# Optimization experiments

Measured on AMD Instinct MI355X. Metric: run time of the kernel, lower is better.

The kernel has to match this reference:

```python
import jax, jax.numpy as jnp
import numpy as np

B, H, C, N, K_TERMS = 256, 512, 64, 100, 8


def eval_cubic_spline(coeffs, tobs, t):
    # coeffs: [B, N-1, 4, C]; tobs: [N] sorted knots; t: scalar
    idx = jnp.clip(jnp.searchsorted(tobs, t, side='right') - 1, 0, tobs.shape[0] - 2)
    dt = t - tobs[idx]
    c = coeffs[:, idx]  # [B, 4, C]
    # Horner evaluation: c0 + c1*dt + c2*dt^2 + c3*dt^3
    return c[:, 0] + dt * (c[:, 1] + dt * (c[:, 2] + dt * c[:, 3]))


def setup_inputs() -> dict:
    key = jax.random.key(0)
    k_h, k_c, k_dc, k_wx, k_wh, k_wo = jax.random.split(key, 6)
    xav = lambda k, shape: jax.random.uniform(
        k, shape, minval=-1.0, maxval=1.0, dtype=jnp.float32
    ) * np.float32(np.sqrt(6.0 / (shape[0] + shape[1])))
    return {
        't': jnp.float32(0.5),
        'h': jax.random.normal(k_h, (B, H), dtype=jnp.float32),
        'coeffs': jax.random.normal(k_c, (B, N - 1, 4, C), dtype=jnp.float32),
        'dcoeffs': jax.random.normal(k_dc, (B, N - 1, 4, C), dtype=jnp.float32),
        'tobs': jnp.linspace(0.0, 1.0, N, dtype=jnp.float32),
        'wx': xav(k_wx, (H, C)),
        'wh': xav(k_wh, (H, H)),
        'wout': xav(k_wo, (H, H)),
        'b0': jnp.zeros((H,), dtype=jnp.float32),
        'b1': jnp.zeros((H,), dtype=jnp.float32),
    }


def reference(t, h, coeffs, dcoeffs, tobs, wx, wh, wout, b0, b1):
    x = eval_cubic_spline(coeffs, tobs, t)      # [B, C]
    xdot = eval_cubic_spline(dcoeffs, tobs, t)  # [B, C]
    l1 = x @ wx.T + h @ wh.T + b0               # [B, H]
    relu = jnp.maximum(l1, 0.0)
    th = jnp.tanh(relu @ wout.T + b1)           # [B, H]
    dtanh = 1.0 - th * th
    drelu = jax.nn.sigmoid(l1)                  # surrogate_relu branch
    # Jacobian assembly via broadcasted outer product: [B, H, H]
    d_outer = dtanh[:, :, None] * wout[None, :, :] * drelu[:, None, :]
    Jx = d_outer @ wx                           # [B, H, C]
    Jh = d_outer @ wh                           # [B, H, H]
    curr = jnp.einsum('bhc,bc->bh', Jx, xdot)   # jx matvec, [B, H]
    h_dot = curr
    for _ in range(K_TERMS):                    # Neumann-series recurrence
        curr = jnp.einsum('bij,bj->bi', Jh, curr)
        h_dot = h_dot + curr
    return h_dot
```

## Files before the change

### kernel.cpp

```cpp
#include <hip/hip_runtime.h>

#define BB 256
#define HH 512
#define CC 64
#define NN 100
#define KT 8

typedef short s16x8 __attribute__((ext_vector_type(8)));
typedef float f32x4 __attribute__((ext_vector_type(4)));

#define MFMA16(a, b, c) __builtin_amdgcn_mfma_f32_16x16x32_bf16((a), (b), (c), 0, 0, 0)

static __device__ __forceinline__ unsigned short f2bf(float f) {
    union { float f; unsigned int u; } v; v.f = f;
    unsigned int r = v.u + 0x7FFFu + ((v.u >> 16) & 1u);
    return (unsigned short)(r >> 16);
}


__global__ void k_pack(const float* __restrict__ wh, const float* __restrict__ wout,
                       const float* __restrict__ wx, const float* __restrict__ h,
                       const float* __restrict__ coeffs, const float* __restrict__ dcoeffs,
                       const float* __restrict__ tobs, const float* __restrict__ tg,
                       unsigned short* __restrict__ whp, unsigned short* __restrict__ wop,
                       unsigned short* __restrict__ wxp, unsigned short* __restrict__ hb,
                       unsigned short* __restrict__ xb, unsigned short* __restrict__ xdb,
                       unsigned int* __restrict__ cnt) {
    int gid = blockIdx.x * 256 + threadIdx.x;
    if (gid < 524288) {
        const float* src = (gid < 262144) ? wh : wout;
        unsigned short* dst = (gid < 262144) ? whp : wop;
        int p = gid & 262143;
        int e = p & 7, lane = (p >> 3) & 63, g = (p >> 9) & 15, cg = (p >> 13) & 1, w = p >> 14;
        int row = w * 32 + cg * 16 + (lane & 15);
        int k = g * 32 + (lane >> 4) * 8 + e;
        dst[p] = f2bf(src[row * HH + k]);
    } else if (gid < 557056) {
        int p = gid - 524288;
        int e = p & 7, lane = (p >> 3) & 63, g = (p >> 9) & 1, cg = (p >> 10) & 1, w = p >> 11;
        int row = w * 32 + cg * 16 + (lane & 15);
        int k = g * 32 + (lane >> 4) * 8 + e;
        wxp[p] = f2bf(wx[row * CC + k]);
    } else if (gid < 688128) {
        int p = gid - 557056;
        hb[p] = f2bf(h[p]);
    } else if (gid < 704512) {
        int p = gid - 688128;
        int b = p >> 6, c = p & 63;
        float t = tg[0];
        int cntv = 0;
        for (int n = 0; n < NN; n++) cntv += (tobs[n] <= t) ? 1 : 0;
        int idx = cntv - 1;
        idx = idx < 0 ? 0 : (idx > NN - 2 ? NN - 2 : idx);
        float dt = t - tobs[idx];
        const float* cb = coeffs + ((size_t)(b * (NN - 1) + idx) * 4) * CC + c;
        float xv = cb[0] + dt * (cb[CC] + dt * (cb[2 * CC] + dt * cb[3 * CC]));
        const float* db = dcoeffs + ((size_t)(b * (NN - 1) + idx) * 4) * CC + c;
        float xd = db[0] + dt * (db[CC] + dt * (db[2 * CC] + dt * db[3 * CC]));
        xb[p] = f2bf(xv);
        xdb[p] = f2bf(xd);
    } else if (gid < 704768) {
        cnt[gid - 704512] = 0u;
    }
}

__global__ void k_l1(const unsigned short* __restrict__ whp, const unsigned short* __restrict__ wxp,
                     const unsigned short* __restrict__ hb, const unsigned short* __restrict__ xb,
                     const unsigned short* __restrict__ xdb, const float* __restrict__ b0g,
                     unsigned short* __restrict__ relu_b, float* __restrict__ drelu_f,
                     unsigned short* __restrict__ s0_b) {
    __shared__ unsigned short sh[32][520];
    __shared__ unsigned short sx[32][72];
    __shared__ unsigned short sxd[32][72];
    int tid = threadIdx.x;
    int b0 = blockIdx.x * 32;
    int it = blockIdx.y;
    for (int idx = tid; idx < 32 * 64; idx += 256) {
        int r = idx >> 6, c8 = idx & 63;
        *(int4*)&sh[r][c8 * 8] = *(const int4*)&hb[(b0 + r) * HH + c8 * 8];
    }
    for (int idx = tid; idx < 32 * 8; idx += 256) {
        int r = idx >> 3, c8 = idx & 7;
        *(int4*)&sx[r][c8 * 8] = *(const int4*)&xb[(b0 + r) * CC + c8 * 8];
        *(int4*)&sxd[r][c8 * 8] = *(const int4*)&xdb[(b0 + r) * CC + c8 * 8];
    }
    __syncthreads();
    int wv = tid >> 6, lane = tid & 63, col = lane & 15, kq = lane >> 4;
    int isub = it * 64 + wv * 16;
    int wpk = isub >> 5, cg = (isub >> 4) & 1;
    f32x4 acc0 = {0.f, 0.f, 0.f, 0.f}, acc1 = {0.f, 0.f, 0.f, 0.f};
    f32x4 vac0 = {0.f, 0.f, 0.f, 0.f}, vac1 = {0.f, 0.f, 0.f, 0.f};
    const s16x8* whfrag = (const s16x8*)whp + (size_t)((wpk * 2 + cg) * 16) * 64 + lane;
#pragma unroll
    for (int g = 0; g < 16; g++) {
        s16x8 bf = whfrag[g * 64];
        s16x8 a0 = *(const s16x8*)&sh[col][g * 32 + kq * 8];
        s16x8 a1 = *(const s16x8*)&sh[16 + col][g * 32 + kq * 8];
        acc0 = MFMA16(a0, bf, acc0);
        acc1 = MFMA16(a1, bf, acc1);
    }
    const s16x8* wxfrag = (const s16x8*)wxp + (size_t)((wpk * 2 + cg) * 2) * 64 + lane;
#pragma unroll
    for (int g = 0; g < 2; g++) {
        s16x8 bf = wxfrag[g * 64];
        s16x8 a0 = *(const s16x8*)&sx[col][g * 32 + kq * 8];
        s16x8 a1 = *(const s16x8*)&sx[16 + col][g * 32 + kq * 8];
        acc0 = MFMA16(a0, bf, acc0);
        acc1 = MFMA16(a1, bf, acc1);
        s16x8 d0 = *(const s16x8*)&sxd[col][g * 32 + kq * 8];
        s16x8 d1 = *(const s16x8*)&sxd[16 + col][g * 32 + kq * 8];
        vac0 = MFMA16(d0, bf, vac0);
        vac1 = MFMA16(d1, bf, vac1);
    }
    int ic = isub + col;
    float bias = b0g[ic];
#pragma unroll
    for (int r = 0; r < 4; r++) {
        int bb = b0 + kq * 4 + r;
        float l1a = acc0[r] + bias;
        float dra = 1.f / (1.f + expf(-l1a));
        relu_b[bb * HH + ic] = f2bf(fmaxf(l1a, 0.f));
        drelu_f[bb * HH + ic] = dra;
        s0_b[bb * HH + ic] = f2bf(dra * vac0[r]);
        float l1b = acc1[r] + bias;
        float drb = 1.f / (1.f + expf(-l1b));
        relu_b[(bb + 16) * HH + ic] = f2bf(fmaxf(l1b, 0.f));
        drelu_f[(bb + 16) * HH + ic] = drb;
        s0_b[(bb + 16) * HH + ic] = f2bf(drb * vac1[r]);
    }
}

__global__ void k_th(const unsigned short* __restrict__ wop, const unsigned short* __restrict__ relu_b,
                     const unsigned short* __restrict__ s0_b, const float* __restrict__ b1g,
                     float* __restrict__ dtanh_f, unsigned short* __restrict__ curr_b,
                     float* __restrict__ curr0_f) {
    __shared__ unsigned short sr[32][520];
    __shared__ unsigned short ss0[32][520];
    int tid = threadIdx.x;
    int b0 = blockIdx.x * 32;
    int it = blockIdx.y;
    for (int idx = tid; idx < 32 * 64; idx += 256) {
        int r = idx >> 6, c8 = idx & 63;
        *(int4*)&sr[r][c8 * 8] = *(const int4*)&relu_b[(b0 + r) * HH + c8 * 8];
        *(int4*)&ss0[r][c8 * 8] = *(const int4*)&s0_b[(b0 + r) * HH + c8 * 8];
    }
    __syncthreads();
    int wv = tid >> 6, lane = tid & 63, col = lane & 15, kq = lane >> 4;
    int isub = it * 64 + wv * 16;
    int wpk = isub >> 5, cg = (isub >> 4) & 1;
    f32x4 acc0 = {0.f, 0.f, 0.f, 0.f}, acc1 = {0.f, 0.f, 0.f, 0.f};
    f32x4 cac0 = {0.f, 0.f, 0.f, 0.f}, cac1 = {0.f, 0.f, 0.f, 0.f};
    const s16x8* wofrag = (const s16x8*)wop + (size_t)((wpk * 2 + cg) * 16) * 64 + lane;
#pragma unroll
    for (int g = 0; g < 16; g++) {
        s16x8 bf = wofrag[g * 64];
        s16x8 a0 = *(const s16x8*)&sr[col][g * 32 + kq * 8];
        s16x8 a1 = *(const s16x8*)&sr[16 + col][g * 32 + kq * 8];
        acc0 = MFMA16(a0, bf, acc0);
        acc1 = MFMA16(a1, bf, acc1);
        s16x8 p0 = *(const s16x8*)&ss0[col][g * 32 + kq * 8];
        s16x8 p1 = *(const s16x8*)&ss0[16 + col][g * 32 + kq * 8];
        cac0 = MFMA16(p0, bf, cac0);
        cac1 = MFMA16(p1, bf, cac1);
    }
    int ic = isub + col;
    float bias = b1g[ic];
    int fc = (ic >> 5) * 512 + (ic & 7) + (((ic >> 3) & 3) << 7);
#pragma unroll
    for (int r = 0; r < 4; r++) {
        int bb = b0 + kq * 4 + r;
        int row8 = (kq * 4 + r) * 8;
        float th_a = tanhf(acc0[r] + bias);
        float dta = 1.f - th_a * th_a;
        float c0a = dta * cac0[r];
        dtanh_f[bb * HH + ic] = dta;
        curr_b[(bb >> 4) * 8192 + fc + row8] = f2bf(c0a);
        curr0_f[bb * HH + ic] = c0a;
        float th_b = tanhf(acc1[r] + bias);
        float dtb = 1.f - th_b * th_b;
        float c0b = dtb * cac1[r];
        dtanh_f[(bb + 16) * HH + ic] = dtb;
        curr_b[((bb + 16) >> 4) * 8192 + fc + row8] = f2bf(c0b);
        curr0_f[(bb + 16) * HH + ic] = c0b;
    }
}

__global__ __launch_bounds__(512) void k_loop3(
    const unsigned short* __restrict__ whp, const unsigned short* __restrict__ wop,
    const unsigned short* __restrict__ curr_b, const float* __restrict__ curr0_f,
    const float* __restrict__ drelu_f, const float* __restrict__ dtanh_f,
    float* __restrict__ outp) {
    __shared__ __align__(16) unsigned short sa[2][8192];
    const int tid = threadIdx.x;
    const int w = tid >> 6, lane = tid & 63;
    const int col2 = lane & 15, kq = lane >> 4;
    const int bt = blockIdx.x;

    {
        const int4* src = (const int4*)(curr_b + (size_t)bt * 8192);
        int4* dst = (int4*)&sa[0][0];
        dst[tid] = src[tid];
        dst[tid + 512] = src[tid + 512];
    }

    float dr[4][4], dt[4][4], hd[4][4];
#pragma unroll
    for (int t = 0; t < 4; t++) {
        const int c = (w * 4 + t) * 16 + col2;
#pragma unroll
        for (int r = 0; r < 4; r++) {
            const int row = bt * 16 + kq * 4 + r;
            dr[t][r] = drelu_f[row * HH + c];
            dt[t][r] = dtanh_f[row * HH + c];
            hd[t][r] = curr0_f[row * HH + c];
        }
    }

    int fb[4];
#pragma unroll
    for (int t = 0; t < 4; t++)
        fb[t] = ((w * 4 + t) >> 1) * 512 + (col2 & 7) + (((t * 2 + (col2 >> 3)) & 3) << 7) + kq * 32;

    const s16x8* wlh = (const s16x8*)whp + (size_t)w * 4096 + lane;
    const s16x8* wlo = (const s16x8*)wop + (size_t)w * 4096 + lane;
    const unsigned short* A0 = &sa[0][lane * 8];
    const unsigned short* A1 = &sa[1][lane * 8];

    __syncthreads();

    for (int p = 0; p < 16; p++) {
        const s16x8* wl = (p & 1) ? wlo : wlh;
        const unsigned short* Ar = (p & 1) ? A1 : A0;
        f32x4 acc[4] = {{0.f, 0.f, 0.f, 0.f}, {0.f, 0.f, 0.f, 0.f},
                        {0.f, 0.f, 0.f, 0.f}, {0.f, 0.f, 0.f, 0.f}};
        s16x8 bfr[2][4];
#pragma unroll
        for (int t = 0; t < 4; t++) bfr[0][t] = wl[t * 1024];
#pragma unroll
        for (int g = 0; g < 16; g++) {
            if (g < 15) {
#pragma unroll
                for (int t = 0; t < 4; t++) bfr[(g + 1) & 1][t] = wl[t * 1024 + (g + 1) * 64];
            }
            const s16x8 a = *(const s16x8*)(Ar + (size_t)g * 512);
#pragma unroll
            for (int t = 0; t < 4; t++) acc[t] = MFMA16(a, bfr[g & 1][t], acc[t]);
        }
        unsigned short* Aw = &sa[(p + 1) & 1][0];
        if (p & 1) {
            if (p < 15) {
#pragma unroll
                for (int t = 0; t < 4; t++)
#pragma unroll
                    for (int r = 0; r < 4; r++) {
                        float v = dt[t][r] * acc[t][r];
                        hd[t][r] += v;
                        Aw[fb[t] + r * 8] = f2bf(v);
                    }
            } else {
#pragma unroll
                for (int t = 0; t < 4; t++)
#pragma unroll
                    for (int r = 0; r < 4; r++) hd[t][r] += dt[t][r] * acc[t][r];
            }
        } else {
#pragma unroll
            for (int t = 0; t < 4; t++)
#pragma unroll
                for (int r = 0; r < 4; r++)
                    Aw[fb[t] + r * 8] = f2bf(dr[t][r] * acc[t][r]);
        }
        if (p < 15) __syncthreads();
    }

#pragma unroll
    for (int t = 0; t < 4; t++) {
        const int c = (w * 4 + t) * 16 + col2;
#pragma unroll
        for (int r = 0; r < 4; r++)
            outp[(size_t)(bt * 16 + kq * 4 + r) * HH + c] = hd[t][r];
    }
}

extern "C" void kernel_launch(void* const* d_in, const int* in_sizes, int n_in,
                              void* d_out, int out_size, void* d_ws, size_t ws_size,
                              hipStream_t stream) {
    const float* tg = (const float*)d_in[0];
    const float* h = (const float*)d_in[1];
    const float* coeffs = (const float*)d_in[2];
    const float* dcoeffs = (const float*)d_in[3];
    const float* tobs = (const float*)d_in[4];
    const float* wx = (const float*)d_in[5];
    const float* wh = (const float*)d_in[6];
    const float* wout = (const float*)d_in[7];
    const float* b0g = (const float*)d_in[8];
    const float* b1g = (const float*)d_in[9];
    float* outp = (float*)d_out;

    char* ws = (char*)d_ws;
    unsigned short* whp    = (unsigned short*)(ws + 0);
    unsigned short* wop    = (unsigned short*)(ws + 524288);
    unsigned short* wxp    = (unsigned short*)(ws + 1048576);
    unsigned short* hb     = (unsigned short*)(ws + 1114112);
    unsigned short* xb     = (unsigned short*)(ws + 1376256);
    unsigned short* xdb    = (unsigned short*)(ws + 1409024);
    unsigned short* relu_b = (unsigned short*)(ws + 1441792);
    unsigned short* s0_b   = (unsigned short*)(ws + 1703936);
    float* drelu_f         = (float*)(ws + 1966080);
    float* dtanh_f         = (float*)(ws + 2490368);
    unsigned short* curr_b = (unsigned short*)(ws + 3014656);
    float* curr0_f         = (float*)(ws + 3276800);
    unsigned int* cnt      = (unsigned int*)(ws + 4063232);

    k_pack<<<2753, 256, 0, stream>>>(wh, wout, wx, h, coeffs, dcoeffs, tobs, tg,
                                     whp, wop, wxp, hb, xb, xdb, cnt);
    k_l1<<<dim3(8, 8), 256, 0, stream>>>(whp, wxp, hb, xb, xdb, b0g, relu_b, drelu_f, s0_b);
    k_th<<<dim3(8, 8), 256, 0, stream>>>(wop, relu_b, s0_b, b1g, dtanh_f, curr_b, curr0_f);
    k_loop3<<<16, 512, 0, stream>>>(whp, wop, curr_b, curr0_f, drelu_f, dtanh_f, outp);
}
```

Measured before the change: 182.0 us.

## Fuse l1 and tanh stages into the Neumann loop kernel

The separate k_l1 and k_th kernels are removed, and their matmuls now run at the start of the loop kernel, each block handling its own 16-row batch tile. Intermediates (relu, s0, curr) stay in shared memory and registers instead of making round trips through global memory, which also drops two kernel launches. The pack kernel now writes h and x/xdot in MFMA fragment order so they can be loaded directly. The trade-off is that the l1 and th stages now run on only 16 blocks instead of 64 each, so those prologue GEMMs get less parallelism.

```diff
diff --git a/kernel.cpp b/kernel.cpp
--- a/kernel.cpp
+++ b/kernel.cpp
@@ -23,9 +23,8 @@
                        const float* __restrict__ coeffs, const float* __restrict__ dcoeffs,
                        const float* __restrict__ tobs, const float* __restrict__ tg,
                        unsigned short* __restrict__ whp, unsigned short* __restrict__ wop,
-                       unsigned short* __restrict__ wxp, unsigned short* __restrict__ hb,
-                       unsigned short* __restrict__ xb, unsigned short* __restrict__ xdb,
-                       unsigned int* __restrict__ cnt) {
+                       unsigned short* __restrict__ wxp, unsigned short* __restrict__ hf,
+                       unsigned short* __restrict__ xf, unsigned short* __restrict__ xdf) {
     int gid = blockIdx.x * 256 + threadIdx.x;
     if (gid < 524288) {
         const float* src = (gid < 262144) ? wh : wout;
@@ -43,7 +42,10 @@
         wxp[p] = f2bf(wx[row * CC + k]);
     } else if (gid < 688128) {
         int p = gid - 557056;
-        hb[p] = f2bf(h[p]);
+        int e = p & 7, lane = (p >> 3) & 63, g = (p >> 9) & 15, btp = p >> 13;
+        int row = btp * 16 + (lane & 15);
+        int k = g * 32 + (lane >> 4) * 8 + e;
+        hf[p] = f2bf(h[row * HH + k]);
     } else if (gid < 704512) {
         int p = gid - 688128;
         int b = p >> 6, c = p & 63;
@@ -57,138 +59,17 @@
         float xv = cb[0] + dt * (cb[CC] + dt * (cb[2 * CC] + dt * cb[3 * CC]));
         const float* db = dcoeffs + ((size_t)(b * (NN - 1) + idx) * 4) * CC + c;
         float xd = db[0] + dt * (db[CC] + dt * (db[2 * CC] + dt * db[3 * CC]));
-        xb[p] = f2bf(xv);
-        xdb[p] = f2bf(xd);
-    } else if (gid < 704768) {
-        cnt[gid - 704512] = 0u;
-    }
-}
-
-__global__ void k_l1(const unsigned short* __restrict__ whp, const unsigned short* __restrict__ wxp,
-                     const unsigned short* __restrict__ hb, const unsigned short* __restrict__ xb,
-                     const unsigned short* __restrict__ xdb, const float* __restrict__ b0g,
-                     unsigned short* __restrict__ relu_b, float* __restrict__ drelu_f,
-                     unsigned short* __restrict__ s0_b) {
-    __shared__ unsigned short sh[32][520];
-    __shared__ unsigned short sx[32][72];
-    __shared__ unsigned short sxd[32][72];
-    int tid = threadIdx.x;
-    int b0 = blockIdx.x * 32;
-    int it = blockIdx.y;
-    for (int idx = tid; idx < 32 * 64; idx += 256) {
-        int r = idx >> 6, c8 = idx & 63;
-        *(int4*)&sh[r][c8 * 8] = *(const int4*)&hb[(b0 + r) * HH + c8 * 8];
-    }
-    for (int idx = tid; idx < 32 * 8; idx += 256) {
-        int r = idx >> 3, c8 = idx & 7;
-        *(int4*)&sx[r][c8 * 8] = *(const int4*)&xb[(b0 + r) * CC + c8 * 8];
-        *(int4*)&sxd[r][c8 * 8] = *(const int4*)&xdb[(b0 + r) * CC + c8 * 8];
-    }
-    __syncthreads();
-    int wv = tid >> 6, lane = tid & 63, col = lane & 15, kq = lane >> 4;
-    int isub = it * 64 + wv * 16;
-    int wpk = isub >> 5, cg = (isub >> 4) & 1;
-    f32x4 acc0 = {0.f, 0.f, 0.f, 0.f}, acc1 = {0.f, 0.f, 0.f, 0.f};
-    f32x4 vac0 = {0.f, 0.f, 0.f, 0.f}, vac1 = {0.f, 0.f, 0.f, 0.f};
-    const s16x8* whfrag = (const s16x8*)whp + (size_t)((wpk * 2 + cg) * 16) * 64 + lane;
-#pragma unroll
-    for (int g = 0; g < 16; g++) {
-        s16x8 bf = whfrag[g * 64];
-        s16x8 a0 = *(const s16x8*)&sh[col][g * 32 + kq * 8];
-        s16x8 a1 = *(const s16x8*)&sh[16 + col][g * 32 + kq * 8];
-        acc0 = MFMA16(a0, bf, acc0);
-        acc1 = MFMA16(a1, bf, acc1);
-    }
-    const s16x8* wxfrag = (const s16x8*)wxp + (size_t)((wpk * 2 + cg) * 2) * 64 + lane;
-#pragma unroll
-    for (int g = 0; g < 2; g++) {
-        s16x8 bf = wxfrag[g * 64];
-        s16x8 a0 = *(const s16x8*)&sx[col][g * 32 + kq * 8];
-        s16x8 a1 = *(const s16x8*)&sx[16 + col][g * 32 + kq * 8];
-        acc0 = MFMA16(a0, bf, acc0);
-        acc1 = MFMA16(a1, bf, acc1);
-        s16x8 d0 = *(const s16x8*)&sxd[col][g * 32 + kq * 8];
-        s16x8 d1 = *(const s16x8*)&sxd[16 + col][g * 32 + kq * 8];
-        vac0 = MFMA16(d0, bf, vac0);
-        vac1 = MFMA16(d1, bf, vac1);
-    }
-    int ic = isub + col;
-    float bias = b0g[ic];
-#pragma unroll
-    for (int r = 0; r < 4; r++) {
-        int bb = b0 + kq * 4 + r;
-        float l1a = acc0[r] + bias;
-        float dra = 1.f / (1.f + expf(-l1a));
-        relu_b[bb * HH + ic] = f2bf(fmaxf(l1a, 0.f));
-        drelu_f[bb * HH + ic] = dra;
-        s0_b[bb * HH + ic] = f2bf(dra * vac0[r]);
-        float l1b = acc1[r] + bias;
-        float drb = 1.f / (1.f + expf(-l1b));
-        relu_b[(bb + 16) * HH + ic] = f2bf(fmaxf(l1b, 0.f));
-        drelu_f[(bb + 16) * HH + ic] = drb;
-        s0_b[(bb + 16) * HH + ic] = f2bf(drb * vac1[r]);
-    }
-}
-
-__global__ void k_th(const unsigned short* __restrict__ wop, const unsigned short* __restrict__ relu_b,
-                     const unsigned short* __restrict__ s0_b, const float* __restrict__ b1g,
-                     float* __restrict__ dtanh_f, unsigned short* __restrict__ curr_b,
-                     float* __restrict__ curr0_f) {
-    __shared__ unsigned short sr[32][520];
-    __shared__ unsigned short ss0[32][520];
-    int tid = threadIdx.x;
-    int b0 = blockIdx.x * 32;
-    int it = blockIdx.y;
-    for (int idx = tid; idx < 32 * 64; idx += 256) {
-        int r = idx >> 6, c8 = idx & 63;
-        *(int4*)&sr[r][c8 * 8] = *(const int4*)&relu_b[(b0 + r) * HH + c8 * 8];
-        *(int4*)&ss0[r][c8 * 8] = *(const int4*)&s0_b[(b0 + r) * HH + c8 * 8];
-    }
-    __syncthreads();
-    int wv = tid >> 6, lane = tid & 63, col = lane & 15, kq = lane >> 4;
-    int isub = it * 64 + wv * 16;
-    int wpk = isub >> 5, cg = (isub >> 4) & 1;
-    f32x4 acc0 = {0.f, 0.f, 0.f, 0.f}, acc1 = {0.f, 0.f, 0.f, 0.f};
-    f32x4 cac0 = {0.f, 0.f, 0.f, 0.f}, cac1 = {0.f, 0.f, 0.f, 0.f};
-    const s16x8* wofrag = (const s16x8*)wop + (size_t)((wpk * 2 + cg) * 16) * 64 + lane;
-#pragma unroll
-    for (int g = 0; g < 16; g++) {
-        s16x8 bf = wofrag[g * 64];
-        s16x8 a0 = *(const s16x8*)&sr[col][g * 32 + kq * 8];
-        s16x8 a1 = *(const s16x8*)&sr[16 + col][g * 32 + kq * 8];
-        acc0 = MFMA16(a0, bf, acc0);
-        acc1 = MFMA16(a1, bf, acc1);
-        s16x8 p0 = *(const s16x8*)&ss0[col][g * 32 + kq * 8];
-        s16x8 p1 = *(const s16x8*)&ss0[16 + col][g * 32 + kq * 8];
-        cac0 = MFMA16(p0, bf, cac0);
-        cac1 = MFMA16(p1, bf, cac1);
-    }
-    int ic = isub + col;
-    float bias = b1g[ic];
-    int fc = (ic >> 5) * 512 + (ic & 7) + (((ic >> 3) & 3) << 7);
-#pragma unroll
-    for (int r = 0; r < 4; r++) {
-        int bb = b0 + kq * 4 + r;
-        int row8 = (kq * 4 + r) * 8;
-        float th_a = tanhf(acc0[r] + bias);
-        float dta = 1.f - th_a * th_a;
-        float c0a = dta * cac0[r];
-        dtanh_f[bb * HH + ic] = dta;
-        curr_b[(bb >> 4) * 8192 + fc + row8] = f2bf(c0a);
-        curr0_f[bb * HH + ic] = c0a;
-        float th_b = tanhf(acc1[r] + bias);
-        float dtb = 1.f - th_b * th_b;
-        float c0b = dtb * cac1[r];
-        dtanh_f[(bb + 16) * HH + ic] = dtb;
-        curr_b[((bb + 16) >> 4) * 8192 + fc + row8] = f2bf(c0b);
-        curr0_f[(bb + 16) * HH + ic] = c0b;
-    }
-}
-
-__global__ __launch_bounds__(512) void k_loop3(
+        int fi = (b >> 4) * 1024 + (c >> 5) * 512 + ((b & 15) + ((c >> 3) & 3) * 16) * 8 + (c & 7);
+        xf[fi] = f2bf(xv);
+        xdf[fi] = f2bf(xd);
+    }
+}
+
+__global__ __launch_bounds__(512) void k_fused(
     const unsigned short* __restrict__ whp, const unsigned short* __restrict__ wop,
-    const unsigned short* __restrict__ curr_b, const float* __restrict__ curr0_f,
-    const float* __restrict__ drelu_f, const float* __restrict__ dtanh_f,
+    const unsigned short* __restrict__ wxp, const unsigned short* __restrict__ hf,
+    const unsigned short* __restrict__ xf, const unsigned short* __restrict__ xdf,
+    const float* __restrict__ b0g, const float* __restrict__ b1g,
     float* __restrict__ outp) {
     __shared__ __align__(16) unsigned short sa[2][8192];
     const int tid = threadIdx.x;
@@ -196,38 +77,106 @@
     const int col2 = lane & 15, kq = lane >> 4;
     const int bt = blockIdx.x;
 
-    {
-        const int4* src = (const int4*)(curr_b + (size_t)bt * 8192);
-        int4* dst = (int4*)&sa[0][0];
-        dst[tid] = src[tid];
-        dst[tid + 512] = src[tid + 512];
-    }
-
-    float dr[4][4], dt[4][4], hd[4][4];
+    float b0v[4], b1v[4];
+    int fb[4];
 #pragma unroll
     for (int t = 0; t < 4; t++) {
         const int c = (w * 4 + t) * 16 + col2;
-#pragma unroll
-        for (int r = 0; r < 4; r++) {
-            const int row = bt * 16 + kq * 4 + r;
-            dr[t][r] = drelu_f[row * HH + c];
-            dt[t][r] = dtanh_f[row * HH + c];
-            hd[t][r] = curr0_f[row * HH + c];
-        }
-    }
-
-    int fb[4];
-#pragma unroll
-    for (int t = 0; t < 4; t++)
+        b0v[t] = b0g[c];
+        b1v[t] = b1g[c];
         fb[t] = ((w * 4 + t) >> 1) * 512 + (col2 & 7) + (((t * 2 + (col2 >> 3)) & 3) << 7) + kq * 32;
+    }
 
     const s16x8* wlh = (const s16x8*)whp + (size_t)w * 4096 + lane;
     const s16x8* wlo = (const s16x8*)wop + (size_t)w * 4096 + lane;
+
+    float dr[4][4], dt[4][4], hd[4][4];
+
+    {
+        const s16x8* ha = (const s16x8*)(hf + (size_t)bt * 8192) + lane;
+        f32x4 acc[4] = {{0.f, 0.f, 0.f, 0.f}, {0.f, 0.f, 0.f, 0.f},
+                        {0.f, 0.f, 0.f, 0.f}, {0.f, 0.f, 0.f, 0.f}};
+        f32x4 vac[4] = {{0.f, 0.f, 0.f, 0.f}, {0.f, 0.f, 0.f, 0.f},
+                        {0.f, 0.f, 0.f, 0.f}, {0.f, 0.f, 0.f, 0.f}};
+        s16x8 bfr[2][4], af[2];
+        af[0] = ha[0];
+#pragma unroll
+        for (int t = 0; t < 4; t++) bfr[0][t] = wlh[t * 1024];
+#pragma unroll
+        for (int g = 0; g < 16; g++) {
+            if (g < 15) {
+                af[(g + 1) & 1] = ha[(g + 1) * 64];
+#pragma unroll
+                for (int t = 0; t < 4; t++) bfr[(g + 1) & 1][t] = wlh[t * 1024 + (g + 1) * 64];
+            }
+#pragma unroll
+            for (int t = 0; t < 4; t++) acc[t] = MFMA16(af[g & 1], bfr[g & 1][t], acc[t]);
+        }
+#pragma unroll
+        for (int g = 0; g < 2; g++) {
+            const s16x8 xa = *((const s16x8*)(xf + (size_t)bt * 1024 + g * 512) + lane);
+            const s16x8 xda = *((const s16x8*)(xdf + (size_t)bt * 1024 + g * 512) + lane);
+#pragma unroll
+            for (int t = 0; t < 4; t++) {
+                const s16x8 bf = ((const s16x8*)wxp)[(size_t)((w * 4 + t) * 2 + g) * 64 + lane];
+                acc[t] = MFMA16(xa, bf, acc[t]);
+                vac[t] = MFMA16(xda, bf, vac[t]);
+            }
+        }
+#pragma unroll
+        for (int t = 0; t < 4; t++)
+#pragma unroll
+            for (int r = 0; r < 4; r++) {
+                const float l1 = acc[t][r] + b0v[t];
+                const float dra = 1.f / (1.f + expf(-l1));
+                dr[t][r] = dra;
+                sa[0][fb[t] + r * 8] = f2bf(fmaxf(l1, 0.f));
+                sa[1][fb[t] + r * 8] = f2bf(dra * vac[t][r]);
+            }
+    }
+    __syncthreads();
+
+    {
+        const unsigned short* A0 = &sa[0][lane * 8];
+        const unsigned short* A1 = &sa[1][lane * 8];
+        f32x4 acc[4] = {{0.f, 0.f, 0.f, 0.f}, {0.f, 0.f, 0.f, 0.f},
+                        {0.f, 0.f, 0.f, 0.f}, {0.f, 0.f, 0.f, 0.f}};
+        f32x4 cac[4] = {{0.f, 0.f, 0.f, 0.f}, {0.f, 0.f, 0.f, 0.f},
+                        {0.f, 0.f, 0.f, 0.f}, {0.f, 0.f, 0.f, 0.f}};
+        s16x8 bfr[2][4];
+#pragma unroll
+        for (int t = 0; t < 4; t++) bfr[0][t] = wlo[t * 1024];
+#pragma unroll
+        for (int g = 0; g < 16; g++) {
+            if (g < 15) {
+#pragma unroll
+                for (int t = 0; t < 4; t++) bfr[(g + 1) & 1][t] = wlo[t * 1024 + (g + 1) * 64];
+            }
+            const s16x8 ar = *(const s16x8*)(A0 + (size_t)g * 512);
+            const s16x8 as = *(const s16x8*)(A1 + (size_t)g * 512);
+#pragma unroll
+            for (int t = 0; t < 4; t++) {
+                acc[t] = MFMA16(ar, bfr[g & 1][t], acc[t]);
+                cac[t] = MFMA16(as, bfr[g & 1][t], cac[t]);
+            }
+        }
+        __syncthreads();
+#pragma unroll
+        for (int t = 0; t < 4; t++)
+#pragma unroll
+            for (int r = 0; r < 4; r++) {
+                const float th = tanhf(acc[t][r] + b1v[t]);
+                const float dtv = 1.f - th * th;
+                dt[t][r] = dtv;
+                const float c0 = dtv * cac[t][r];
+                hd[t][r] = c0;
+                sa[0][fb[t] + r * 8] = f2bf(c0);
+            }
+    }
+    __syncthreads();
+
     const unsigned short* A0 = &sa[0][lane * 8];
     const unsigned short* A1 = &sa[1][lane * 8];
-
-    __syncthreads();
-
     for (int p = 0; p < 16; p++) {
         const s16x8* wl = (p & 1) ? wlo : wlh;
         const unsigned short* Ar = (p & 1) ? A1 : A0;
@@ -298,23 +247,14 @@
     float* outp = (float*)d_out;
 
     char* ws = (char*)d_ws;
-    unsigned short* whp    = (unsigned short*)(ws + 0);
-    unsigned short* wop    = (unsigned short*)(ws + 524288);
-    unsigned short* wxp    = (unsigned short*)(ws + 1048576);
-    unsigned short* hb     = (unsigned short*)(ws + 1114112);
-    unsigned short* xb     = (unsigned short*)(ws + 1376256);
-    unsigned short* xdb    = (unsigned short*)(ws + 1409024);
-    unsigned short* relu_b = (unsigned short*)(ws + 1441792);
-    unsigned short* s0_b   = (unsigned short*)(ws + 1703936);
-    float* drelu_f         = (float*)(ws + 1966080);
-    float* dtanh_f         = (float*)(ws + 2490368);
-    unsigned short* curr_b = (unsigned short*)(ws + 3014656);
-    float* curr0_f         = (float*)(ws + 3276800);
-    unsigned int* cnt      = (unsigned int*)(ws + 4063232);
-
-    k_pack<<<2753, 256, 0, stream>>>(wh, wout, wx, h, coeffs, dcoeffs, tobs, tg,
-                                     whp, wop, wxp, hb, xb, xdb, cnt);
-    k_l1<<<dim3(8, 8), 256, 0, stream>>>(whp, wxp, hb, xb, xdb, b0g, relu_b, drelu_f, s0_b);
-    k_th<<<dim3(8, 8), 256, 0, stream>>>(wop, relu_b, s0_b, b1g, dtanh_f, curr_b, curr0_f);
-    k_loop3<<<16, 512, 0, stream>>>(whp, wop, curr_b, curr0_f, drelu_f, dtanh_f, outp);
-}
+    unsigned short* whp = (unsigned short*)(ws + 0);
+    unsigned short* wop = (unsigned short*)(ws + 524288);
+    unsigned short* wxp = (unsigned short*)(ws + 1048576);
+    unsigned short* hf  = (unsigned short*)(ws + 1114112);
+    unsigned short* xf  = (unsigned short*)(ws + 1376256);
+    unsigned short* xdf = (unsigned short*)(ws + 1409024);
+
+    k_pack<<<2752, 256, 0, stream>>>(wh, wout, wx, h, coeffs, dcoeffs, tobs, tg,
+                                     whp, wop, wxp, hf, xf, xdf);
+    k_fused<<<16, 512, 0, stream>>>(whp, wop, wxp, hf, xf, xdf, b0g, b1g, outp);
+}
```

Result: slower. 189.8 us (+4.3%).

## Double warps in Neumann loop, pin last weight slice in LDS, pipeline across phases

Applied to the files above, without the earlier changes.

The recurrence kernel moves from 8 to 16 waves per block. Each wave now owns 2 column tiles instead of 4, which halves per-wave MFMA work and register use. The last K-slice of both weight matrices is copied into shared memory so that its MFMA can run first while global loads for the next phase's first slices are prefetched. The phase loop is restructured into a macro with cross-phase double-buffered weight fragments, and an unused counter buffer clear is dropped from the pack kernel. The trade-off is more LDS use and more waves contending at each barrier.

```diff
diff --git a/kernel.cpp b/kernel.cpp
--- a/kernel.cpp
+++ b/kernel.cpp
@@ -24,8 +24,7 @@
                        const float* __restrict__ tobs, const float* __restrict__ tg,
                        unsigned short* __restrict__ whp, unsigned short* __restrict__ wop,
                        unsigned short* __restrict__ wxp, unsigned short* __restrict__ hb,
-                       unsigned short* __restrict__ xb, unsigned short* __restrict__ xdb,
-                       unsigned int* __restrict__ cnt) {
+                       unsigned short* __restrict__ xb, unsigned short* __restrict__ xdb) {
     int gid = blockIdx.x * 256 + threadIdx.x;
     if (gid < 524288) {
         const float* src = (gid < 262144) ? wh : wout;
@@ -59,8 +58,6 @@
         float xd = db[0] + dt * (db[CC] + dt * (db[2 * CC] + dt * db[3 * CC]));
         xb[p] = f2bf(xv);
         xdb[p] = f2bf(xd);
-    } else if (gid < 704768) {
-        cnt[gid - 704512] = 0u;
     }
 }
 
@@ -185,12 +182,34 @@
     }
 }
 
-__global__ __launch_bounds__(512) void k_loop3(
+#define PHASE(WL, WLN, PIN, XORc, AR) do {                                     \
+    _Pragma("unroll") for (int t = 0; t < 2; t++) acc[t] = (f32x4){0.f,0.f,0.f,0.f}; \
+    {                                                                          \
+        const s16x8 a15 = *(const s16x8*)((AR) + 15 * 512);                    \
+        _Pragma("unroll") for (int t = 0; t < 2; t++)                          \
+            acc[t] = MFMA16(a15, (PIN)[t * 64], acc[t]);                       \
+    }                                                                          \
+    _Pragma("unroll")                                                          \
+    for (int g = 0; g < 15; g++) {                                             \
+        const s16x8 a = *(const s16x8*)((AR) + g * 512);                       \
+        const int bi = (g & 1) ^ (XORc);                                       \
+        _Pragma("unroll") for (int t = 0; t < 2; t++)                          \
+            acc[t] = MFMA16(a, bfr[bi][t], acc[t]);                            \
+        const s16x8* ws = (g < 13) ? (WL) : (WLN);                             \
+        const int gg = (g < 13) ? (g + 2) : (g - 13);                          \
+        _Pragma("unroll") for (int t = 0; t < 2; t++)                          \
+            bfr[bi][t] = ws[t * 1024 + gg * 64];                               \
+    }                                                                          \
+} while (0)
+
+__global__ __launch_bounds__(1024, 4) void k_loop4(
     const unsigned short* __restrict__ whp, const unsigned short* __restrict__ wop,
     const unsigned short* __restrict__ curr_b, const float* __restrict__ curr0_f,
     const float* __restrict__ drelu_f, const float* __restrict__ dtanh_f,
     float* __restrict__ outp) {
     __shared__ __align__(16) unsigned short sa[2][8192];
+    __shared__ __align__(16) unsigned short wpinh[16384];
+    __shared__ __align__(16) unsigned short wpino[16384];
     const int tid = threadIdx.x;
     const int w = tid >> 6, lane = tid & 63;
     const int col2 = lane & 15, kq = lane >> 4;
@@ -198,15 +217,24 @@
 
     {
         const int4* src = (const int4*)(curr_b + (size_t)bt * 8192);
-        int4* dst = (int4*)&sa[0][0];
-        dst[tid] = src[tid];
-        dst[tid + 512] = src[tid + 512];
-    }
-
-    float dr[4][4], dt[4][4], hd[4][4];
-#pragma unroll
-    for (int t = 0; t < 4; t++) {
-        const int c = (w * 4 + t) * 16 + col2;
+        ((int4*)&sa[0][0])[tid] = src[tid];
+    }
+    {
+        const int4* s0 = (const int4*)whp;
+        const int4* s1 = (const int4*)wop;
+        int4* d0 = (int4*)wpinh;
+        int4* d1 = (int4*)wpino;
+        for (int i = tid; i < 2048; i += 1024) {
+            const int srcIdx = (i >> 6) * 1024 + 15 * 64 + (i & 63);
+            d0[i] = s0[srcIdx];
+            d1[i] = s1[srcIdx];
+        }
+    }
+
+    float dr[2][4], dt[2][4], hd[2][4];
+#pragma unroll
+    for (int t = 0; t < 2; t++) {
+        const int c = (w * 2 + t) * 16 + col2;
 #pragma unroll
         for (int r = 0; r < 4; r++) {
             const int row = bt * 16 + kq * 4 + r;
@@ -215,67 +243,61 @@
             hd[t][r] = curr0_f[row * HH + c];
         }
     }
-
-    int fb[4];
-#pragma unroll
-    for (int t = 0; t < 4; t++)
-        fb[t] = ((w * 4 + t) >> 1) * 512 + (col2 & 7) + (((t * 2 + (col2 >> 3)) & 3) << 7) + kq * 32;
-
-    const s16x8* wlh = (const s16x8*)whp + (size_t)w * 4096 + lane;
-    const s16x8* wlo = (const s16x8*)wop + (size_t)w * 4096 + lane;
+    int fb[2];
+#pragma unroll
+    for (int t = 0; t < 2; t++) {
+        const int ct = w * 2 + t;
+        fb[t] = (ct >> 1) * 512 + (col2 & 7) + ((((ct & 1) * 2 + (col2 >> 3)) & 3) << 7) + kq * 32;
+    }
+
+    const s16x8* wlh = (const s16x8*)whp + (size_t)(w * 2) * 1024 + lane;
+    const s16x8* wlo = (const s16x8*)wop + (size_t)(w * 2) * 1024 + lane;
     const unsigned short* A0 = &sa[0][lane * 8];
     const unsigned short* A1 = &sa[1][lane * 8];
+    const s16x8* pinh = (const s16x8*)&wpinh[0] + (size_t)(w * 2) * 64 + lane;
+    const s16x8* pino = (const s16x8*)&wpino[0] + (size_t)(w * 2) * 64 + lane;
+
+    f32x4 acc[2];
+    s16x8 bfr[2][2];
+#pragma unroll
+    for (int t = 0; t < 2; t++) {
+        bfr[0][t] = wlh[t * 1024 + 0 * 64];
+        bfr[1][t] = wlh[t * 1024 + 1 * 64];
+    }
 
     __syncthreads();
 
-    for (int p = 0; p < 16; p++) {
-        const s16x8* wl = (p & 1) ? wlo : wlh;
-        const unsigned short* Ar = (p & 1) ? A1 : A0;
-        f32x4 acc[4] = {{0.f, 0.f, 0.f, 0.f}, {0.f, 0.f, 0.f, 0.f},
-                        {0.f, 0.f, 0.f, 0.f}, {0.f, 0.f, 0.f, 0.f}};
-        s16x8 bfr[2][4];
-#pragma unroll
-        for (int t = 0; t < 4; t++) bfr[0][t] = wl[t * 1024];
-#pragma unroll
-        for (int g = 0; g < 16; g++) {
-            if (g < 15) {
-#pragma unroll
-                for (int t = 0; t < 4; t++) bfr[(g + 1) & 1][t] = wl[t * 1024 + (g + 1) * 64];
-            }
-            const s16x8 a = *(const s16x8*)(Ar + (size_t)g * 512);
-#pragma unroll
-            for (int t = 0; t < 4; t++) acc[t] = MFMA16(a, bfr[g & 1][t], acc[t]);
+    for (int it = 0; it < 8; it++) {
+        PHASE(wlh, wlo, pinh, 0, A0);
+#pragma unroll
+        for (int t = 0; t < 2; t++)
+#pragma unroll
+            for (int r = 0; r < 4; r++)
+                sa[1][fb[t] + r * 8] = f2bf(dr[t][r] * acc[t][r]);
+        __syncthreads();
+
+        PHASE(wlo, wlh, pino, 1, A1);
+        if (it < 7) {
+#pragma unroll
+            for (int t = 0; t < 2; t++)
+#pragma unroll
+                for (int r = 0; r < 4; r++) {
+                    const float v = dt[t][r] * acc[t][r];
+                    hd[t][r] += v;
+                    sa[0][fb[t] + r * 8] = f2bf(v);
+                }
+            __syncthreads();
+        } else {
+#pragma unroll
+            for (int t = 0; t < 2; t++)
+#pragma unroll
+                for (int r = 0; r < 4; r++) hd[t][r] += dt[t][r] * acc[t][r];
         }
-        unsigned short* Aw = &sa[(p + 1) & 1][0];
-        if (p & 1) {
-            if (p < 15) {
-#pragma unroll
-                for (int t = 0; t < 4; t++)
-#pragma unroll
-                    for (int r = 0; r < 4; r++) {
-                        float v = dt[t][r] * acc[t][r];
-                        hd[t][r] += v;
-                        Aw[fb[t] + r * 8] = f2bf(v);
-                    }
-            } else {
-#pragma unroll
-                for (int t = 0; t < 4; t++)
-#pragma unroll
-                    for (int r = 0; r < 4; r++) hd[t][r] += dt[t][r] * acc[t][r];
-            }
-        } else {
-#pragma unroll
-            for (int t = 0; t < 4; t++)
-#pragma unroll
-                for (int r = 0; r < 4; r++)
-                    Aw[fb[t] + r * 8] = f2bf(dr[t][r] * acc[t][r]);
-        }
-        if (p < 15) __syncthreads();
-    }
-
-#pragma unroll
-    for (int t = 0; t < 4; t++) {
-        const int c = (w * 4 + t) * 16 + col2;
+    }
+
+#pragma unroll
+    for (int t = 0; t < 2; t++) {
+        const int c = (w * 2 + t) * 16 + col2;
 #pragma unroll
         for (int r = 0; r < 4; r++)
             outp[(size_t)(bt * 16 + kq * 4 + r) * HH + c] = hd[t][r];
@@ -310,11 +332,10 @@
     float* dtanh_f         = (float*)(ws + 2490368);
     unsigned short* curr_b = (unsigned short*)(ws + 3014656);
     float* curr0_f         = (float*)(ws + 3276800);
-    unsigned int* cnt      = (unsigned int*)(ws + 4063232);
-
-    k_pack<<<2753, 256, 0, stream>>>(wh, wout, wx, h, coeffs, dcoeffs, tobs, tg,
-                                     whp, wop, wxp, hb, xb, xdb, cnt);
+
+    k_pack<<<2752, 256, 0, stream>>>(wh, wout, wx, h, coeffs, dcoeffs, tobs, tg,
+                                     whp, wop, wxp, hb, xb, xdb);
     k_l1<<<dim3(8, 8), 256, 0, stream>>>(whp, wxp, hb, xb, xdb, b0g, relu_b, drelu_f, s0_b);
     k_th<<<dim3(8, 8), 256, 0, stream>>>(wop, relu_b, s0_b, b1g, dtanh_f, curr_b, curr0_f);
-    k_loop3<<<16, 512, 0, stream>>>(whp, wop, curr_b, curr0_f, drelu_f, dtanh_f, outp);
-}
+    k_loop4<<<16, 1024, 0, stream>>>(whp, wop, curr_b, curr0_f, drelu_f, dtanh_f, outp);
+}
```

Measured after the change: 329.1 us. 1.81x slower.
